# Kernel optimization log

Measured on AMD Instinct MI355X. Metric: run time of the kernel, lower is better.

The kernel has to match this reference:

```python
import jax, jax.numpy as jnp
import numpy as np

NHEAD = 16
D_MODEL = 1024
DK = D_MODEL // NHEAD
Q_DIM = V_DIM = K_DIM = 1024
B, S = 2, 2048


def _xavier(key, shape):
    # xavier_uniform over last two dims (fan_in=shape[-2], fan_out=shape[-1])
    fan_in, fan_out = shape[-2], shape[-1]
    limit = float(np.sqrt(6.0 / (fan_in + fan_out)))
    return jax.random.uniform(key, shape, jnp.float32, -limit, limit)


def setup_inputs() -> dict:
    key = jax.random.key(0)
    kq, kv, kk, kwq, kwv, kwk = jax.random.split(key, 6)
    q = jax.random.normal(kq, (B, S, Q_DIM), jnp.float32)
    v = jax.random.normal(kv, (B, S, V_DIM), jnp.float32)
    k = jax.random.normal(kk, (B, S, K_DIM), jnp.float32)
    # causal mask: True = attend, matches masked_fill(~mask, -inf)
    causal = jnp.tril(jnp.ones((S, S), dtype=bool))
    attn_mask = jnp.broadcast_to(causal, (B, S, S))
    q_proj_mats = _xavier(kwq, (NHEAD, Q_DIM, DK))
    v_proj_mats = _xavier(kwv, (NHEAD, V_DIM, DK))
    k_proj_mats = _xavier(kwk, (NHEAD, K_DIM, DK))
    return {"q": q, "v": v, "k": k, "attn_mask": attn_mask,
            "q_proj_mats": q_proj_mats, "v_proj_mats": v_proj_mats,
            "k_proj_mats": k_proj_mats}


def reference(q, v, k, attn_mask, q_proj_mats, v_proj_mats, k_proj_mats):
    bsz, seq_len, _ = q.shape
    # per-head projections: [B,S,dim] x [H,dim,dk] -> [B,H,S,dk]
    qp = jnp.einsum('bsk,hkd->bhsd', q, q_proj_mats)
    vp = jnp.einsum('bsk,hkd->bhsd', v, v_proj_mats)
    kp = jnp.einsum('bsk,hkd->bhsd', k, k_proj_mats)
    # NOTE: original scales by sqrt(d_model), not sqrt(dk)
    scale = 1.0 / jnp.sqrt(jnp.float32(D_MODEL))
    logits = jnp.einsum('bhqd,bhkd->bhqk', qp, kp) * scale  # [B,H,S,S]
    logits = jnp.where(attn_mask[:, None, :, :], logits, -jnp.inf)
    score = jax.nn.softmax(logits, axis=-1)
    weighted = jnp.einsum('bhkd,bhqk->bqhd', vp, score)  # [B,S,H,dk]
    return weighted.reshape(bsz, seq_len, -1)
```

## Files before the change

### kernel.cpp

```cpp
#include <hip/hip_runtime.h>
#include <cstdint>
#include <cstddef>

#define NB 2
#define NS 2048
#define NH 16
#define NDK 64
#define NDM 1024
#define SCALE 0.03125f

using u16 = unsigned short;
typedef __attribute__((ext_vector_type(8))) short bf16x8;
typedef __attribute__((ext_vector_type(4))) float f32x4;

#define AS1 __attribute__((address_space(1)))
#define AS3 __attribute__((address_space(3)))

__device__ __forceinline__ u16 f2bf(float f) {
    unsigned int x = __float_as_uint(f);
    return (u16)((x + 0x7FFFu + ((x >> 16) & 1u)) >> 16);
}
__device__ __forceinline__ unsigned int packbf(float f0, float f1) {
    return __builtin_amdgcn_perm(__float_as_uint(f1), __float_as_uint(f0),
                                 0x07060302u);
}

__global__ __launch_bounds__(256)
void prep(const float* __restrict__ q, const float* __restrict__ v,
          const float* __restrict__ kkk,
          const float* __restrict__ qw, const float* __restrict__ vw,
          const float* __restrict__ kw,
          u16* __restrict__ xt, u16* __restrict__ wbt, int nxblk)
{
    __shared__ __align__(16) u16 SH[64 * 72];
    const int t = threadIdx.x;
    const int bid = blockIdx.x;
    if (bid < nxblk) {
        int z   = bid >> 7;
        int rem = bid & 127;
        int mt  = rem >> 2;
        int kq  = rem & 3;
        const float* X = (z == 0) ? q : (z == 1) ? v : kkk;
        const float* src = X + (size_t)mt * 128 * NDM;
        u16* dst = xt + (((size_t)z * 32 + mt) << 17);
        const int row = t >> 3;
        const int cl  = (t & 7) * 4;
        const int pl  = (t & 7) >> 1;
        const int hf  = (t & 1) * 4;
        for (int kk = kq * 8; kk < kq * 8 + 8; ++kk) {
            #pragma unroll
            for (int i = 0; i < 4; ++i) {
                int ml = row + 32 * i;
                float4 f = *reinterpret_cast<const float4*>(
                    src + (size_t)ml * NDM + kk * 32 + cl);
                uint2 u;
                u.x = packbf(f.x, f.y);
                u.y = packbf(f.z, f.w);
                *reinterpret_cast<uint2*>(&SH[(pl * 128 + ml) * 8 + hf]) = u;
            }
            __syncthreads();
            {
                uint4 o0 = *reinterpret_cast<uint4*>(&SH[(2 * t) * 8]);
                uint4 o1 = *reinterpret_cast<uint4*>(&SH[(2 * t + 1) * 8]);
                u16* dd = dst + ((size_t)kk << 12) + 2 * t * 8;
                *reinterpret_cast<uint4*>(dd)     = o0;
                *reinterpret_cast<uint4*>(dd + 8) = o1;
            }
            __syncthreads();
        }
    } else {
        int b  = bid - nxblk;
        int z  = b >> 8;
        int h  = (b >> 4) & 15;
        int k0 = (b & 15) * 64;
        const float* W = ((z == 0) ? qw : (z == 1) ? vw : kw)
                         + (size_t)h * NDM * NDK;
        {
            int kr = t >> 2, d0 = (t & 3) * 16;
            const float* src = W + (size_t)(k0 + kr) * NDK + d0;
            #pragma unroll
            for (int c = 0; c < 4; ++c) {
                float4 f = *reinterpret_cast<const float4*>(src + c * 4);
                SH[(d0 + c * 4 + 0) * 72 + kr] = f2bf(f.x);
                SH[(d0 + c * 4 + 1) * 72 + kr] = f2bf(f.y);
                SH[(d0 + c * 4 + 2) * 72 + kr] = f2bf(f.z);
                SH[(d0 + c * 4 + 3) * 72 + kr] = f2bf(f.w);
            }
        }
        __syncthreads();
        {
            int pl = t >> 6, d = t & 63;
            int nt = h >> 1;
            int cb = pl * 128 + (h & 1) * 64 + d;
            #pragma unroll
            for (int ki = 0; ki < 2; ++ki) {
                uint4 val = *reinterpret_cast<const uint4*>(
                    &SH[d * 72 + ki * 32 + pl * 8]);
                size_t base = (((size_t)z * 8 + nt) * 32 + (k0 >> 5) + ki) << 12;
                *reinterpret_cast<uint4*>(wbt + base + cb * 8) = val;
            }
        }
    }
}

__device__ __forceinline__ void gemm_epilogue(
    f32x4 acc[4][4], int z, int m0, int n0, int wm, int wn,
    int quad, int l15, u16* __restrict__ O)
{
    const int bb = m0 >> 11;
    const int hh = (n0 + wn) >> 6;
    const size_t headT = ((size_t)(bb * NH + hh)) << 17;
    if (z == 2) {
        #pragma unroll
        for (int mi = 0; mi < 4; ++mi) {
            #pragma unroll
            for (int r = 0; r < 4; ++r) {
                int s = (m0 + wm + mi * 16 + quad * 4 + r) & 2047;
                size_t tb = headT + ((size_t)(s >> 6) << 12) + (s & 63) * 8 + (l15 & 7);
                int chb = l15 >> 3;
                #pragma unroll
                for (int ni = 0; ni < 4; ++ni)
                    O[tb + (ni * 2 + chb) * 512] = f2bf(acc[mi][ni][r]);
            }
        }
    } else if (z == 1) {
        #pragma unroll
        for (int mi = 0; mi < 4; ++mi) {
            #pragma unroll
            for (int r = 0; r < 4; ++r) {
                int s = (m0 + wm + mi * 16 + quad * 4 + r) & 2047;
                size_t tb = headT + ((size_t)(s >> 6) << 12)
                          + ((s & 63) >> 3) * 512 + (s & 7);
                #pragma unroll
                for (int ni = 0; ni < 4; ++ni)
                    O[tb + (ni * 16 + l15) * 8] = f2bf(acc[mi][ni][r]);
            }
        }
    } else {
        #pragma unroll
        for (int mi = 0; mi < 4; ++mi) {
            #pragma unroll
            for (int r = 0; r < 4; ++r) {
                int s = (m0 + wm + mi * 16 + quad * 4 + r) & 2047;
                size_t rb = ((size_t)(bb * NH + hh) * NS + s) * NDK;
                #pragma unroll
                for (int ni = 0; ni < 4; ++ni)
                    O[rb + ni * 16 + l15] = f2bf(acc[mi][ni][r]);
            }
        }
    }
}

__global__ __launch_bounds__(256)
void gemm_xt(const u16* __restrict__ xt, const u16* __restrict__ wbt,
             u16* __restrict__ qp, u16* __restrict__ vp,
             u16* __restrict__ kp)
{
    __shared__ __align__(16) u16 SA[2][4096];
    __shared__ __align__(16) u16 SB[2][4096];

    const int t    = threadIdx.x;
    const int lane = t & 63;
    const int w    = t >> 6;
    const int quad = lane >> 4, l15 = lane & 15;
    const int mt = blockIdx.x, nt = blockIdx.y, z = blockIdx.z;

    const u16* As = xt + (((size_t)z * 32 + mt) << 17);
    const u16* Bs = wbt + (((size_t)z * 8 + nt) << 17);
    u16* O = (z == 0) ? qp : (z == 1) ? vp : kp;
    const int wm = (w & 1) * 64, wn = (w >> 1) * 64;

    #pragma unroll
    for (int i = 0; i < 2; ++i) {
        int c = i * 256 + t;
        __builtin_amdgcn_global_load_lds((const AS1 void*)(As + c * 8),
                                         (AS3 void*)&SA[0][c * 8], 16, 0, 0);
        __builtin_amdgcn_global_load_lds((const AS1 void*)(Bs + c * 8),
                                         (AS3 void*)&SB[0][c * 8], 16, 0, 0);
    }

    f32x4 acc[4][4] = {};

    #pragma unroll 2
    for (int kk = 0; kk < 32; ++kk) {
        const int cur = kk & 1;
        __syncthreads();
        if (kk < 31) {
            const size_t off = (size_t)(kk + 1) << 12;
            #pragma unroll
            for (int i = 0; i < 2; ++i) {
                int c = i * 256 + t;
                __builtin_amdgcn_global_load_lds(
                    (const AS1 void*)(As + off + c * 8),
                    (AS3 void*)&SA[cur ^ 1][c * 8], 16, 0, 0);
                __builtin_amdgcn_global_load_lds(
                    (const AS1 void*)(Bs + off + c * 8),
                    (AS3 void*)&SB[cur ^ 1][c * 8], 16, 0, 0);
            }
        }
        bf16x8 af[4], bfr[4];
        #pragma unroll
        for (int mi = 0; mi < 4; ++mi)
            af[mi] = *reinterpret_cast<const bf16x8*>(
                &SA[cur][quad * 1024 + (wm + mi * 16 + l15) * 8]);
        #pragma unroll
        for (int ni = 0; ni < 4; ++ni)
            bfr[ni] = *reinterpret_cast<const bf16x8*>(
                &SB[cur][quad * 1024 + (wn + ni * 16 + l15) * 8]);
        #pragma unroll
        for (int mi = 0; mi < 4; ++mi)
            #pragma unroll
            for (int ni = 0; ni < 4; ++ni)
                acc[mi][ni] = __builtin_amdgcn_mfma_f32_16x16x32_bf16(
                    af[mi], bfr[ni], acc[mi][ni], 0, 0, 0);
    }

    gemm_epilogue(acc, z, mt * 128, nt * 128, wm, wn, quad, l15, O);
}

__global__ __launch_bounds__(256)
void gemm_pack(const float* __restrict__ q, const float* __restrict__ v,
               const float* __restrict__ kkk, const u16* __restrict__ wbt,
               u16* __restrict__ qp, u16* __restrict__ vp,
               u16* __restrict__ kp)
{
    __shared__ __align__(16) u16 SA[2][4096];
    __shared__ __align__(16) u16 SB[2][4096];

    const int t    = threadIdx.x;
    const int lane = t & 63;
    const int w    = t >> 6;
    const int quad = lane >> 4, l15 = lane & 15;
    const int m0 = blockIdx.x * 128;
    const int n0 = blockIdx.y * 128;
    const int z  = blockIdx.z;

    const float* X = (z == 0) ? q : (z == 1) ? v : kkk;
    const u16* Wb2 = wbt + (((size_t)z * 8 + (n0 >> 7)) << 17);
    u16* O = (z == 0) ? qp : (z == 1) ? vp : kp;

    const int wm = (w & 1) * 64, wn = (w >> 1) * 64;
    const int arow = t >> 3;
    const int acol = (t & 7) * 4;
    const int apl  = (t & 7) >> 1;
    const int aj   = (t & 1) * 4;
    const float* xa = X + (size_t)(m0 + arow) * NDM + acol;

    float4 fA[4];
    #pragma unroll
    for (int i = 0; i < 4; ++i)
        fA[i] = *reinterpret_cast<const float4*>(xa + (size_t)(32 * i) * NDM);
    #pragma unroll
    for (int i = 0; i < 2; ++i) {
        int c = i * 256 + t;
        __builtin_amdgcn_global_load_lds((const AS1 void*)(Wb2 + c * 8),
                                         (AS3 void*)&SB[0][c * 8], 16, 0, 0);
    }

    f32x4 acc[4][4] = {};

    #pragma unroll 2
    for (int kk = 0; kk < 32; ++kk) {
        const int cur = kk & 1;
        #pragma unroll
        for (int i = 0; i < 4; ++i) {
            uint2 u;
            u.x = packbf(fA[i].x, fA[i].y);
            u.y = packbf(fA[i].z, fA[i].w);
            *reinterpret_cast<uint2*>(
                &SA[cur][apl * 1024 + (arow + 32 * i) * 8 + aj]) = u;
        }
        __syncthreads();

        if (kk < 31) {
            const int kn = (kk + 1) * 32;
            const float* p = xa + kn;
            #pragma unroll
            for (int i = 0; i < 4; ++i)
                fA[i] = *reinterpret_cast<const float4*>(p + (size_t)(32 * i) * NDM);
            const u16* src = Wb2 + ((size_t)(kk + 1) << 12);
            #pragma unroll
            for (int i = 0; i < 2; ++i) {
                int c = i * 256 + t;
                __builtin_amdgcn_global_load_lds((const AS1 void*)(src + c * 8),
                                                 (AS3 void*)&SB[cur ^ 1][c * 8], 16, 0, 0);
            }
        }

        bf16x8 af[4], bfr[4];
        #pragma unroll
        for (int mi = 0; mi < 4; ++mi)
            af[mi] = *reinterpret_cast<const bf16x8*>(
                &SA[cur][quad * 1024 + (wm + mi * 16 + l15) * 8]);
        #pragma unroll
        for (int ni = 0; ni < 4; ++ni)
            bfr[ni] = *reinterpret_cast<const bf16x8*>(
                &SB[cur][quad * 1024 + (wn + ni * 16 + l15) * 8]);
        #pragma unroll
        for (int mi = 0; mi < 4; ++mi)
            #pragma unroll
            for (int ni = 0; ni < 4; ++ni)
                acc[mi][ni] = __builtin_amdgcn_mfma_f32_16x16x32_bf16(
                    af[mi], bfr[ni], acc[mi][ni], 0, 0, 0);
    }

    gemm_epilogue(acc, z, m0, n0, wm, wn, quad, l15, O);
}

__global__ __launch_bounds__(256)
void attn_kernel(const u16* __restrict__ QP, const u16* __restrict__ KP,
                 const u16* __restrict__ VT, float* __restrict__ Out)
{
    __shared__ __align__(16) u16 KB[2][4096];
    __shared__ __align__(16) u16 VB[2][4096];
    __shared__ __align__(16) u16 Pl[4][2][16 * 64];

    const int t    = threadIdx.x;
    const int w    = t >> 6;
    const int lane = t & 63;
    const int quad = lane >> 4, l15 = lane & 15;

    const int pi = blockIdx.x & 15;
    const int bh = blockIdx.x >> 4;
    const int qtA = 31 - pi, qtB = pi;
    const size_t headQ = (size_t)bh * NS * NDK;
    const size_t headT = (size_t)bh << 17;
    const int q0A = qtA * 64 + w * 16, q0B = qtB * 64 + w * 16;

    bf16x8 qfA0, qfA1, qfB0, qfB1;
    {
        const u16* qa = QP + headQ + (size_t)(q0A + l15) * NDK + quad * 8;
        qfA0 = *reinterpret_cast<const bf16x8*>(qa);
        qfA1 = *reinterpret_cast<const bf16x8*>(qa + 32);
        const u16* qb = QP + headQ + (size_t)(q0B + l15) * NDK + quad * 8;
        qfB0 = *reinterpret_cast<const bf16x8*>(qb);
        qfB1 = *reinterpret_cast<const bf16x8*>(qb + 32);
    }

    f32x4 oA[4] = {}, oB[4] = {};
    float lA[4] = {}, lB[4] = {};

    const int SrowW = ((quad & 3) << 1);
    const int SrowR = (((l15 >> 2) & 3) << 1);

    #pragma unroll
    for (int i = 0; i < 2; ++i) {
        int c = i * 256 + t;
        __builtin_amdgcn_global_load_lds((const AS1 void*)(KP + headT + c * 8),
                                         (AS3 void*)&KB[0][c * 8], 16, 0, 0);
        __builtin_amdgcn_global_load_lds((const AS1 void*)(VT + headT + c * 8),
                                         (AS3 void*)&VB[0][c * 8], 16, 0, 0);
    }

    for (int kt = 0; kt <= qtA; ++kt) {
        const int cur = kt & 1;
        __syncthreads();
        if (kt < qtA) {
            const int nb = cur ^ 1;
            const size_t tb = headT + ((size_t)(kt + 1) << 12);
            #pragma unroll
            for (int i = 0; i < 2; ++i) {
                int c = i * 256 + t;
                __builtin_amdgcn_global_load_lds((const AS1 void*)(KP + tb + c * 8),
                                                 (AS3 void*)&KB[nb][c * 8], 16, 0, 0);
                __builtin_amdgcn_global_load_lds((const AS1 void*)(VT + tb + c * 8),
                                                 (AS3 void*)&VB[nb][c * 8], 16, 0, 0);
            }
        }

        const bool doB = (kt <= qtB);
        const bool dA = (kt == qtA), dB = (kt == qtB);

        f32x4 sA[4], sB[4];
        #pragma unroll
        for (int g = 0; g < 4; ++g) {
            const int rowoff = (g * 16 + l15) * 8;
            bf16x8 k0 = *reinterpret_cast<const bf16x8*>(&KB[cur][quad * 512 + rowoff]);
            bf16x8 k1 = *reinterpret_cast<const bf16x8*>(&KB[cur][(quad + 4) * 512 + rowoff]);
            f32x4 z = {};
            sA[g] = __builtin_amdgcn_mfma_f32_16x16x32_bf16(qfA1, k1,
                      __builtin_amdgcn_mfma_f32_16x16x32_bf16(qfA0, k0, z, 0, 0, 0),
                      0, 0, 0);
            if (doB)
                sB[g] = __builtin_amdgcn_mfma_f32_16x16x32_bf16(qfB1, k1,
                          __builtin_amdgcn_mfma_f32_16x16x32_bf16(qfB0, k0, z, 0, 0, 0),
                          0, 0, 0);
        }

        #pragma unroll
        for (int g = 0; g < 4; ++g) {
            int key = kt * 64 + g * 16 + l15;
            int ph  = ((g * 16 + l15) >> 3) ^ SrowW;
            int base = ph * 8 + (l15 & 7);
            #pragma unroll
            for (int r = 0; r < 4; ++r) {
                float p = __expf(sA[g][r] * SCALE);
                if (dA && key > q0A + quad * 4 + r) p = 0.0f;
                lA[r] += p;
                Pl[w][0][(quad * 4 + r) * 64 + base] =
                    (u16)((__float_as_uint(p) + 0x8000u) >> 16);
            }
        }
        if (doB) {
            #pragma unroll
            for (int g = 0; g < 4; ++g) {
                int key = kt * 64 + g * 16 + l15;
                int ph  = ((g * 16 + l15) >> 3) ^ SrowW;
                int base = ph * 8 + (l15 & 7);
                #pragma unroll
                for (int r = 0; r < 4; ++r) {
                    float p = __expf(sB[g][r] * SCALE);
                    if (dB && key > q0B + quad * 4 + r) p = 0.0f;
                    lB[r] += p;
                    Pl[w][1][(quad * 4 + r) * 64 + base] =
                        (u16)((__float_as_uint(p) + 0x8000u) >> 16);
                }
            }
        }

        const int pc0 = (quad ^ SrowR) * 8;
        const int pc1 = ((quad + 4) ^ SrowR) * 8;
        bf16x8 pA0 = *reinterpret_cast<const bf16x8*>(&Pl[w][0][l15 * 64 + pc0]);
        bf16x8 pA1 = *reinterpret_cast<const bf16x8*>(&Pl[w][0][l15 * 64 + pc1]);
        bf16x8 pB0, pB1;
        if (doB) {
            pB0 = *reinterpret_cast<const bf16x8*>(&Pl[w][1][l15 * 64 + pc0]);
            pB1 = *reinterpret_cast<const bf16x8*>(&Pl[w][1][l15 * 64 + pc1]);
        }
        #pragma unroll
        for (int d = 0; d < 4; ++d) {
            const int rowoff = (d * 16 + l15) * 8;
            bf16x8 v0 = *reinterpret_cast<const bf16x8*>(&VB[cur][quad * 512 + rowoff]);
            bf16x8 v1 = *reinterpret_cast<const bf16x8*>(&VB[cur][(quad + 4) * 512 + rowoff]);
            oA[d] = __builtin_amdgcn_mfma_f32_16x16x32_bf16(pA1, v1,
                      __builtin_amdgcn_mfma_f32_16x16x32_bf16(pA0, v0, oA[d], 0, 0, 0),
                      0, 0, 0);
            if (doB)
                oB[d] = __builtin_amdgcn_mfma_f32_16x16x32_bf16(pB1, v1,
                          __builtin_amdgcn_mfma_f32_16x16x32_bf16(pB0, v0, oB[d], 0, 0, 0),
                          0, 0, 0);
        }
    }

    #pragma unroll
    for (int off = 1; off < 16; off <<= 1) {
        #pragma unroll
        for (int r = 0; r < 4; ++r) {
            lA[r] += __shfl_xor(lA[r], off, 64);
            lB[r] += __shfl_xor(lB[r], off, 64);
        }
    }

    const int bb = bh >> 4, h = bh & 15;
    #pragma unroll
    for (int r = 0; r < 4; ++r) {
        float ia = 1.0f / lA[r], ib = 1.0f / lB[r];
        size_t oa = ((size_t)bb * NS + q0A + quad * 4 + r) * NDM + h * 64 + l15;
        size_t ob = ((size_t)bb * NS + q0B + quad * 4 + r) * NDM + h * 64 + l15;
        #pragma unroll
        for (int d = 0; d < 4; ++d) {
            Out[oa + d * 16] = oA[d][r] * ia;
            Out[ob + d * 16] = oB[d][r] * ib;
        }
    }
}

extern "C" void kernel_launch(void* const* d_in, const int* in_sizes, int n_in,
                              void* d_out, int out_size, void* d_ws, size_t ws_size,
                              hipStream_t stream) {
    const float* q  = (const float*)d_in[0];
    const float* v  = (const float*)d_in[1];
    const float* k  = (const float*)d_in[2];
    const float* qw = (const float*)d_in[4];
    const float* vw = (const float*)d_in[5];
    const float* kw = (const float*)d_in[6];

    const size_t PSZ = (size_t)NB * NH * NS * NDK;
    u16* wbt = (u16*)d_ws;
    u16* qp  = wbt + (size_t)3 * NDM * NDM;
    u16* vp  = qp + PSZ;
    u16* kp  = vp + PSZ;
    u16* xt  = kp + PSZ;

    const size_t NEED_XT = ((size_t)3 * NDM * NDM + 3 * PSZ
                            + (size_t)3 * 4096 * NDM) * 2;
    const bool xtpath = (ws_size >= NEED_XT);
    const int nx = xtpath ? 384 : 0;

    prep<<<dim3(768 + nx), dim3(256), 0, stream>>>(
        q, v, k, qw, vw, kw, xtpath ? xt : (u16*)d_ws, wbt, nx);

    if (xtpath)
        gemm_xt<<<dim3(32, 8, 3), dim3(256), 0, stream>>>(xt, wbt, qp, vp, kp);
    else
        gemm_pack<<<dim3(32, 8, 3), dim3(256), 0, stream>>>(q, v, k, wbt,
                                                            qp, vp, kp);

    attn_kernel<<<dim3(32 * 16), dim3(256), 0, stream>>>(qp, kp, vp,
                                                         (float*)d_out);
}
```

Measured before the change: 207.3 us.

## Split paired query tiles into separate blocks and transpose score MFMA

The attention kernel no longer pairs a long and a short query tile per block. It launches one block per query tile (1024 blocks), ordered heaviest-first so the causal imbalance is handled by the scheduler. The QK MFMA operands are swapped so each lane holds four consecutive keys for one query row, which allows packed 8-byte P stores into a new XOR swizzle and a single per-lane row sum with fewer shuffles. In exchange, K/V tiles are loaded once per query tile instead of being shared by two tiles, which increases L2/global traffic.

```diff
diff --git a/kernel.cpp b/kernel.cpp
--- a/kernel.cpp
+++ b/kernel.cpp
@@ -313,35 +313,30 @@
 {
     __shared__ __align__(16) u16 KB[2][4096];
     __shared__ __align__(16) u16 VB[2][4096];
-    __shared__ __align__(16) u16 Pl[4][2][16 * 64];
+    __shared__ __align__(16) u16 Pl[4][1024];
 
     const int t    = threadIdx.x;
     const int w    = t >> 6;
     const int lane = t & 63;
     const int quad = lane >> 4, l15 = lane & 15;
 
-    const int pi = blockIdx.x & 15;
-    const int bh = blockIdx.x >> 4;
-    const int qtA = 31 - pi, qtB = pi;
+    const int qt = 31 - (blockIdx.x >> 5);
+    const int bh = blockIdx.x & 31;
     const size_t headQ = (size_t)bh * NS * NDK;
     const size_t headT = (size_t)bh << 17;
-    const int q0A = qtA * 64 + w * 16, q0B = qtB * 64 + w * 16;
-
-    bf16x8 qfA0, qfA1, qfB0, qfB1;
+    const int q0 = qt * 64 + w * 16;
+
+    bf16x8 qf0, qf1;
     {
-        const u16* qa = QP + headQ + (size_t)(q0A + l15) * NDK + quad * 8;
-        qfA0 = *reinterpret_cast<const bf16x8*>(qa);
-        qfA1 = *reinterpret_cast<const bf16x8*>(qa + 32);
-        const u16* qb = QP + headQ + (size_t)(q0B + l15) * NDK + quad * 8;
-        qfB0 = *reinterpret_cast<const bf16x8*>(qb);
-        qfB1 = *reinterpret_cast<const bf16x8*>(qb + 32);
-    }
-
-    f32x4 oA[4] = {}, oB[4] = {};
-    float lA[4] = {}, lB[4] = {};
-
-    const int SrowW = ((quad & 3) << 1);
-    const int SrowR = (((l15 >> 2) & 3) << 1);
+        const u16* qa = QP + headQ + (size_t)(q0 + l15) * NDK + quad * 8;
+        qf0 = *reinterpret_cast<const bf16x8*>(qa);
+        qf1 = *reinterpret_cast<const bf16x8*>(qa + 32);
+    }
+
+    f32x4 o[4] = {};
+    float lsum = 0.0f;
+
+    const int swz = (l15 & 3) << 4;
 
     #pragma unroll
     for (int i = 0; i < 2; ++i) {
@@ -352,10 +347,10 @@
                                          (AS3 void*)&VB[0][c * 8], 16, 0, 0);
     }
 
-    for (int kt = 0; kt <= qtA; ++kt) {
+    for (int kt = 0; kt <= qt; ++kt) {
         const int cur = kt & 1;
         __syncthreads();
-        if (kt < qtA) {
+        if (kt < qt) {
             const int nb = cur ^ 1;
             const size_t tb = headT + ((size_t)(kt + 1) << 12);
             #pragma unroll
@@ -368,100 +363,68 @@
             }
         }
 
-        const bool doB = (kt <= qtB);
-        const bool dA = (kt == qtA), dB = (kt == qtB);
-
-        f32x4 sA[4], sB[4];
+        f32x4 s[4];
         #pragma unroll
         for (int g = 0; g < 4; ++g) {
             const int rowoff = (g * 16 + l15) * 8;
             bf16x8 k0 = *reinterpret_cast<const bf16x8*>(&KB[cur][quad * 512 + rowoff]);
             bf16x8 k1 = *reinterpret_cast<const bf16x8*>(&KB[cur][(quad + 4) * 512 + rowoff]);
             f32x4 z = {};
-            sA[g] = __builtin_amdgcn_mfma_f32_16x16x32_bf16(qfA1, k1,
-                      __builtin_amdgcn_mfma_f32_16x16x32_bf16(qfA0, k0, z, 0, 0, 0),
-                      0, 0, 0);
-            if (doB)
-                sB[g] = __builtin_amdgcn_mfma_f32_16x16x32_bf16(qfB1, k1,
-                          __builtin_amdgcn_mfma_f32_16x16x32_bf16(qfB0, k0, z, 0, 0, 0),
-                          0, 0, 0);
-        }
-
+            s[g] = __builtin_amdgcn_mfma_f32_16x16x32_bf16(k1, qf1,
+                     __builtin_amdgcn_mfma_f32_16x16x32_bf16(k0, qf0, z, 0, 0, 0),
+                     0, 0, 0);
+        }
+
+        const bool diag = (kt == qt);
         #pragma unroll
         for (int g = 0; g < 4; ++g) {
-            int key = kt * 64 + g * 16 + l15;
-            int ph  = ((g * 16 + l15) >> 3) ^ SrowW;
-            int base = ph * 8 + (l15 & 7);
-            #pragma unroll
-            for (int r = 0; r < 4; ++r) {
-                float p = __expf(sA[g][r] * SCALE);
-                if (dA && key > q0A + quad * 4 + r) p = 0.0f;
-                lA[r] += p;
-                Pl[w][0][(quad * 4 + r) * 64 + base] =
-                    (u16)((__float_as_uint(p) + 0x8000u) >> 16);
-            }
-        }
-        if (doB) {
-            #pragma unroll
-            for (int g = 0; g < 4; ++g) {
-                int key = kt * 64 + g * 16 + l15;
-                int ph  = ((g * 16 + l15) >> 3) ^ SrowW;
-                int base = ph * 8 + (l15 & 7);
-                #pragma unroll
-                for (int r = 0; r < 4; ++r) {
-                    float p = __expf(sB[g][r] * SCALE);
-                    if (dB && key > q0B + quad * 4 + r) p = 0.0f;
-                    lB[r] += p;
-                    Pl[w][1][(quad * 4 + r) * 64 + base] =
-                        (u16)((__float_as_uint(p) + 0x8000u) >> 16);
-                }
-            }
-        }
-
-        const int pc0 = (quad ^ SrowR) * 8;
-        const int pc1 = ((quad + 4) ^ SrowR) * 8;
-        bf16x8 pA0 = *reinterpret_cast<const bf16x8*>(&Pl[w][0][l15 * 64 + pc0]);
-        bf16x8 pA1 = *reinterpret_cast<const bf16x8*>(&Pl[w][0][l15 * 64 + pc1]);
-        bf16x8 pB0, pB1;
-        if (doB) {
-            pB0 = *reinterpret_cast<const bf16x8*>(&Pl[w][1][l15 * 64 + pc0]);
-            pB1 = *reinterpret_cast<const bf16x8*>(&Pl[w][1][l15 * 64 + pc1]);
-        }
+            float p0 = __expf(s[g][0] * SCALE);
+            float p1 = __expf(s[g][1] * SCALE);
+            float p2 = __expf(s[g][2] * SCALE);
+            float p3 = __expf(s[g][3] * SCALE);
+            if (diag) {
+                const int kb = g * 16 + quad * 4;
+                const int qr = w * 16 + l15;
+                if (kb + 0 > qr) p0 = 0.0f;
+                if (kb + 1 > qr) p1 = 0.0f;
+                if (kb + 2 > qr) p2 = 0.0f;
+                if (kb + 3 > qr) p3 = 0.0f;
+            }
+            lsum += (p0 + p1) + (p2 + p3);
+            uint2 u;
+            u.x = packbf(p0, p1);
+            u.y = packbf(p2, p3);
+            *reinterpret_cast<uint2*>(
+                &Pl[w][l15 * 64 + ((g * 16 + quad * 4) ^ swz)]) = u;
+        }
+        asm volatile("" ::: "memory");
+
+        bf16x8 pa0 = *reinterpret_cast<const bf16x8*>(
+            &Pl[w][l15 * 64 + ((quad * 8) ^ swz)]);
+        bf16x8 pa1 = *reinterpret_cast<const bf16x8*>(
+            &Pl[w][l15 * 64 + ((32 + quad * 8) ^ swz)]);
         #pragma unroll
         for (int d = 0; d < 4; ++d) {
             const int rowoff = (d * 16 + l15) * 8;
             bf16x8 v0 = *reinterpret_cast<const bf16x8*>(&VB[cur][quad * 512 + rowoff]);
             bf16x8 v1 = *reinterpret_cast<const bf16x8*>(&VB[cur][(quad + 4) * 512 + rowoff]);
-            oA[d] = __builtin_amdgcn_mfma_f32_16x16x32_bf16(pA1, v1,
-                      __builtin_amdgcn_mfma_f32_16x16x32_bf16(pA0, v0, oA[d], 0, 0, 0),
-                      0, 0, 0);
-            if (doB)
-                oB[d] = __builtin_amdgcn_mfma_f32_16x16x32_bf16(pB1, v1,
-                          __builtin_amdgcn_mfma_f32_16x16x32_bf16(pB0, v0, oB[d], 0, 0, 0),
-                          0, 0, 0);
-        }
-    }
-
-    #pragma unroll
-    for (int off = 1; off < 16; off <<= 1) {
-        #pragma unroll
-        for (int r = 0; r < 4; ++r) {
-            lA[r] += __shfl_xor(lA[r], off, 64);
-            lB[r] += __shfl_xor(lB[r], off, 64);
-        }
-    }
+            o[d] = __builtin_amdgcn_mfma_f32_16x16x32_bf16(pa1, v1,
+                     __builtin_amdgcn_mfma_f32_16x16x32_bf16(pa0, v0, o[d], 0, 0, 0),
+                     0, 0, 0);
+        }
+    }
+
+    lsum += __shfl_xor(lsum, 16, 64);
+    lsum += __shfl_xor(lsum, 32, 64);
 
     const int bb = bh >> 4, h = bh & 15;
     #pragma unroll
     for (int r = 0; r < 4; ++r) {
-        float ia = 1.0f / lA[r], ib = 1.0f / lB[r];
-        size_t oa = ((size_t)bb * NS + q0A + quad * 4 + r) * NDM + h * 64 + l15;
-        size_t ob = ((size_t)bb * NS + q0B + quad * 4 + r) * NDM + h * 64 + l15;
-        #pragma unroll
-        for (int d = 0; d < 4; ++d) {
-            Out[oa + d * 16] = oA[d][r] * ia;
-            Out[ob + d * 16] = oB[d][r] * ib;
-        }
+        float inv = 1.0f / __shfl(lsum, quad * 4 + r, 64);
+        size_t ob = ((size_t)bb * NS + q0 + quad * 4 + r) * NDM + h * 64 + l15;
+        #pragma unroll
+        for (int d = 0; d < 4; ++d)
+            Out[ob + d * 16] = o[d][r] * inv;
     }
 }
 
@@ -496,6 +459,6 @@
         gemm_pack<<<dim3(32, 8, 3), dim3(256), 0, stream>>>(q, v, k, wbt,
                                                             qp, vp, kp);
 
-    attn_kernel<<<dim3(32 * 16), dim3(256), 0, stream>>>(qp, kp, vp,
+    attn_kernel<<<dim3(32 * 32), dim3(256), 0, stream>>>(qp, kp, vp,
                                                          (float*)d_out);
 }
```

Result: faster. 197.4 us (-4.8%).
